# Kernel optimization log

Hardware: AMD Instinct MI355X
Metric: run time of the kernel (lower is better)

Reference implementation:

```python
import jax, jax.numpy as jnp
import numpy as np

D_EMBEDDING = 512
DIMENSION = 64
B, N = 8, 2048


def setup_inputs() -> dict:
    key = jax.random.key(0)
    k1, k2, k3, k4, k5, k6 = jax.random.split(key, 6)
    bound = 1.0 / np.sqrt(D_EMBEDDING)  # nn.Linear default init
    return {
        "key_input": jax.random.normal(k1, (B, N, D_EMBEDDING), jnp.float32),
        "query_input": jax.random.normal(k2, (B, N, D_EMBEDDING), jnp.float32),
        "value_input": jax.random.normal(k3, (B, N, D_EMBEDDING), jnp.float32),
        "padding_mask": jnp.zeros((B, 1, N), dtype=bool),
        "masked_attention": 1,
        "W_key": jax.random.uniform(k4, (D_EMBEDDING, DIMENSION), jnp.float32, -bound, bound),
        "W_query": jax.random.uniform(k5, (D_EMBEDDING, DIMENSION), jnp.float32, -bound, bound),
        "W_value": jax.random.uniform(k6, (D_EMBEDDING, DIMENSION), jnp.float32, -bound, bound),
    }


def reference(key_input, query_input, value_input, padding_mask, masked_attention,
              W_key, W_query, W_value):
    # NOTE: faithful to the original torch code, which uses self.key for
    # Q, K AND V (W_query / W_value are unused by forward) and scales by
    # sqrt(D_i) where D_i is the INPUT embedding dim (512), not the head dim.
    B_, N_, D_i = value_input.shape
    K = key_input @ W_key      # [B, N, d]
    Q = query_input @ W_key    # [B, N, d]
    V = value_input @ W_key    # [B, N, d]

    scores = jnp.einsum("bqd,bkd->bqk", Q, K) / jnp.sqrt(jnp.float32(D_i))
    neg_inf = jnp.float32(-jnp.inf)
    scores = jnp.where(padding_mask, neg_inf, scores)
    if masked_attention:
        causal = jnp.tril(jnp.ones((N_, N_), dtype=bool))  # [N, N]
        scores = jnp.where(causal, scores, neg_inf)
    probs = jax.nn.softmax(scores, axis=-1)
    return jnp.einsum("bqk,bkd->bqd", probs, V)
```

## Files before the change

### kernel.cpp

```cpp
#include <hip/hip_runtime.h>
#include <hip/hip_bf16.h>
#include <math.h>

#define D_EMB 512
#define HD 64
#define BB 8
#define NN 2048
#define MROWS (BB*NN)

typedef short short8  __attribute__((ext_vector_type(8)));
typedef short short4v __attribute__((ext_vector_type(4)));
typedef float f32x4   __attribute__((ext_vector_type(4)));

#define QSCALE 0.063758708f

__device__ __forceinline__ short f2bf(float x){
    unsigned u = __float_as_uint(x);
    unsigned r = (u + 0x7fffu + ((u >> 16) & 1u)) >> 16;
    return (short)r;
}
__device__ __forceinline__ float bf2f(short b){
    return __uint_as_float(((unsigned)(unsigned short)b) << 16);
}
__device__ __forceinline__ unsigned pkbf(float a, float b){
    __hip_bfloat162 h = __float22bfloat162_rn(make_float2(a, b));
    unsigned u; __builtin_memcpy(&u, &h, 4); return u;
}
__device__ __forceinline__ void gl16(const short* g, short* l){
    __builtin_amdgcn_global_load_lds(
        (const __attribute__((address_space(1))) unsigned*)g,
        (__attribute__((address_space(3))) unsigned*)l, 16, 0, 0);
}

__global__ __launch_bounds__(256)
void wt_kernel(const float* __restrict__ W, short* __restrict__ Wtf){
    for (int idx = blockIdx.x * 256 + threadIdx.x; idx < D_EMB*HD; idx += 8*256){
        int k = idx >> 6, n = idx & 63;
        int off = (((k >> 5)*4 + (n >> 4))*64 + ((k >> 3) & 3)*16 + (n & 15))*8 + (k & 7);
        Wtf[off] = f2bf(W[idx]);
    }
}

__global__ __launch_bounds__(256, 4)
void proj_kernel(const float* __restrict__ Xq, const float* __restrict__ Xk,
                 const float* __restrict__ Xv, const short* __restrict__ Wtf,
                 short* __restrict__ Qb, short* __restrict__ Kb,
                 short* __restrict__ Vt)
{
    const int tid = threadIdx.x;
    const int lane = tid & 63;
    const int lc = lane & 15, quad = lane >> 4;
    const int wid = blockIdx.x * 4 + (tid >> 6);
    const int m0 = wid * 16;
    const int tensor = m0 >> 14;
    const int rloc = m0 & (MROWS - 1);
    const float* X = (tensor == 0) ? Xq : (tensor == 1 ? Xk : Xv);
    const float* xbase = X + (size_t)(rloc + lc)*D_EMB + quad*8;

    f32x4 acc[4];
#pragma unroll
    for (int t = 0; t < 4; ++t)
#pragma unroll
        for (int r = 0; r < 4; ++r) acc[t][r] = 0.f;

    float4 xa[4][2];
#pragma unroll
    for (int p = 0; p < 4; ++p){
        xa[p][0] = *(const float4*)(xbase + p*32);
        xa[p][1] = *(const float4*)(xbase + p*32 + 4);
    }
#pragma unroll
    for (int c16 = 0; c16 < 16; ++c16){
        float4 f0 = xa[c16 & 3][0], f1 = xa[c16 & 3][1];
        if (c16 < 12){
            xa[c16 & 3][0] = *(const float4*)(xbase + (c16+4)*32);
            xa[c16 & 3][1] = *(const float4*)(xbase + (c16+4)*32 + 4);
        }
        union { short8 s8; unsigned u[4]; } a;
        a.u[0] = pkbf(f0.x, f0.y); a.u[1] = pkbf(f0.z, f0.w);
        a.u[2] = pkbf(f1.x, f1.y); a.u[3] = pkbf(f1.z, f1.w);
#pragma unroll
        for (int t = 0; t < 4; ++t){
            short8 bf = *(const short8*)(Wtf + (size_t)(((c16*4 + t)*64 + lane)*8));
            acc[t] = __builtin_amdgcn_mfma_f32_16x16x32_bf16(a.s8, bf, acc[t], 0,0,0);
        }
    }

    if (tensor == 0){
#pragma unroll
        for (int t = 0; t < 4; ++t)
#pragma unroll
            for (int r = 0; r < 4; ++r)
                Qb[(size_t)(rloc + quad*4 + r)*HD + t*16 + lc] = f2bf(acc[t][r] * QSCALE);
    } else if (tensor == 1){
#pragma unroll
        for (int t = 0; t < 4; ++t)
#pragma unroll
            for (int r = 0; r < 4; ++r){
                const int R = rloc + quad*4 + r;
                const int nin = R & 63;
                const int off = ((R >> 6) << 12) + nin*64
                              + ((((t << 1) | (lc >> 3)) ^ (nin & 7)) << 3) + (lc & 7);
                Kb[off] = f2bf(acc[t][r]);
            }
    } else {
#pragma unroll
        for (int t = 0; t < 4; ++t)
#pragma unroll
            for (int r = 0; r < 4; ++r){
                const int R = rloc + quad*4 + r;
                const int nin = R & 63;
                const int d = t*16 + lc;
                const int off = ((R >> 6) << 12) + d*64
                              + (((nin >> 3) ^ (lc & 7)) << 3) + (nin & 7);
                Vt[off] = f2bf(acc[t][r]);
            }
    }
}

template<int SH>
__global__ __launch_bounds__(256)
void attn_part(const short* __restrict__ Qb, const short* __restrict__ Kb,
               const short* __restrict__ Vt, const unsigned char* __restrict__ pad,
               const int* __restrict__ mflag, float* __restrict__ out,
               float* __restrict__ Lp, short* __restrict__ Op)
{
    constexpr int M   = 1 << SH;
    constexpr int NG  = 32 / M;
    constexpr int UPB = M * NG * (NG + 1) / 2;
    constexpr int PPB = UPB - M;

    __shared__ short sK[2][4096];
    __shared__ short sV[2][4096];
    __shared__ short sP[4][16][80];

    const int tid = threadIdx.x, lane = tid & 63, lc = lane & 15, quad = lane >> 4, w = tid >> 6;
    const int unit = blockIdx.x;
    const int b = unit / UPB;
    const int rem = unit - b * UPB;
    int a = 0;
    while (rem >= (M * (a + 1) * (a + 2)) / 2) ++a;
    const int u = rem - M * a * (a + 1) / 2;
    const int C = a + 1;
    const int r = u / C, c = u - r * C;
    const int j = a * M + r;
    const int q0 = j * 64;

    const bool causal = (mflag[0] != 0);
    const int T = causal ? (j + 1) : 32;
    const int qq = (T + C - 1) / C;
    const int t0 = c * qq;
    const int t1 = min(t0 + qq, T);
    const int tb = b * 32;
    const unsigned char* padb = pad + (size_t)b * NN;

    const short* qrow = Qb + ((size_t)b * NN + q0 + w*16 + lc) * HD;
    const short8 qf0 = *(const short8*)(qrow + quad * 8);
    const short8 qf1 = *(const short8*)(qrow + 32 + quad * 8);

    f32x4 o[4];
#pragma unroll
    for (int t = 0; t < 4; ++t)
#pragma unroll
        for (int rr = 0; rr < 4; ++rr) o[t][rr] = 0.f;
    float lacc = 0.f;

    {
        const short* gk = Kb + ((size_t)(tb + t0) << 12) + w*1024 + lane*8;
        const short* gv = Vt + ((size_t)(tb + t0) << 12) + w*1024 + lane*8;
        short* lk = &sK[0][w*1024 + lane*8];
        short* lv = &sV[0][w*1024 + lane*8];
        gl16(gk, lk); gl16(gk + 512, lk + 512);
        gl16(gv, lv); gl16(gv + 512, lv + 512);
    }

    int buf = 0;
    const int sw = lc & 7;
    for (int kt = t0; kt < t1; ++kt, buf ^= 1){
        __syncthreads();
        if (kt + 1 < t1){
            const short* gk = Kb + ((size_t)(tb + kt + 1) << 12) + w*1024 + lane*8;
            const short* gv = Vt + ((size_t)(tb + kt + 1) << 12) + w*1024 + lane*8;
            short* lk = &sK[buf ^ 1][w*1024 + lane*8];
            short* lv = &sV[buf ^ 1][w*1024 + lane*8];
            gl16(gk, lk); gl16(gk + 512, lk + 512);
            gl16(gv, lv); gl16(gv + 512, lv + 512);
        }
        const int k0 = kt * 64;
        short8 kf0[4], kf1[4], vf0[4], vf1[4];
#pragma unroll
        for (int t = 0; t < 4; ++t){
            const int row = (t*16 + lc) * 64;
            kf0[t] = *(const short8*)&sK[buf][row + ((quad ^ sw) << 3)];
            kf1[t] = *(const short8*)&sK[buf][row + (((quad + 4) ^ sw) << 3)];
            vf0[t] = *(const short8*)&sV[buf][row + ((quad ^ sw) << 3)];
            vf1[t] = *(const short8*)&sV[buf][row + (((quad + 4) ^ sw) << 3)];
        }
        f32x4 st[4];
#pragma unroll
        for (int t = 0; t < 4; ++t){
#pragma unroll
            for (int rr = 0; rr < 4; ++rr) st[t][rr] = 0.f;
            st[t] = __builtin_amdgcn_mfma_f32_16x16x32_bf16(kf0[t], qf0, st[t], 0,0,0);
            st[t] = __builtin_amdgcn_mfma_f32_16x16x32_bf16(kf1[t], qf1, st[t], 0,0,0);
        }
        const bool dg = causal && (kt == j);
        const int thr = q0 + w*16 + lc - k0;
#pragma unroll
        for (int t = 0; t < 4; ++t){
            uchar4 pb = *(const uchar4*)(padb + k0 + t*16 + quad*4);
            float e[4];
#pragma unroll
            for (int rr = 0; rr < 4; ++rr){
                float v = st[t][rr];
                const unsigned char pr = (rr==0)?pb.x:(rr==1)?pb.y:(rr==2)?pb.z:pb.w;
                const int nloc = t*16 + quad*4 + rr;
                if (pr || (dg && nloc > thr)) v = -INFINITY;
                e[rr] = exp2f(v);
                lacc += e[rr];
            }
            union { short4v s4; unsigned uu[2]; } pk;
            pk.uu[0] = pkbf(e[0], e[1]);
            pk.uu[1] = pkbf(e[2], e[3]);
            *(short4v*)&sP[w][lc][t*16 + quad*4] = pk.s4;
        }
        const short8 pf0 = *(const short8*)&sP[w][lc][quad*8];
        const short8 pf1 = *(const short8*)&sP[w][lc][32 + quad*8];
#pragma unroll
        for (int t = 0; t < 4; ++t){
            o[t] = __builtin_amdgcn_mfma_f32_16x16x32_bf16(pf0, vf0[t], o[t], 0,0,0);
            o[t] = __builtin_amdgcn_mfma_f32_16x16x32_bf16(pf1, vf1[t], o[t], 0,0,0);
        }
    }

    lacc += __shfl_xor(lacc, 16);
    lacc += __shfl_xor(lacc, 32);

    if (C == 1){
        float linv[4];
#pragma unroll
        for (int rr = 0; rr < 4; ++rr) linv[rr] = 1.f / __shfl(lacc, quad*4 + rr);
#pragma unroll
        for (int rr = 0; rr < 4; ++rr){
            float* orow = out + ((size_t)b*NN + q0 + w*16 + quad*4 + rr)*HD;
#pragma unroll
            for (int t = 0; t < 4; ++t) orow[t*16 + lc] = o[t][rr] * linv[rr];
        }
    } else {
        const int pu = b*PPB + (M*a*(a+1)/2 - M) + r*C + c;
        short* op = Op + (size_t)pu * 4096;
#pragma unroll
        for (int t = 0; t < 4; ++t)
#pragma unroll
            for (int rr = 0; rr < 4; ++rr)
                op[(w*16 + quad*4 + rr)*64 + t*16 + lc] = f2bf(o[t][rr]);
        if (lane < 16) Lp[pu*64 + w*16 + lane] = lacc;
    }
}

template<int SH>
__global__ __launch_bounds__(256)
void attn_combine(const float* __restrict__ Lp, const short* __restrict__ Op,
                  float* __restrict__ out)
{
    constexpr int M    = 1 << SH;
    constexpr int UPB  = M * (32/M) * (32/M + 1) / 2;
    constexpr int PPB  = UPB - M;
    constexpr int NSTR = 32 - M;
    const int tid = threadIdx.x, lane = tid & 63;
    const int unit = blockIdx.x;
    const int per_b = NSTR * 16;
    const int b = unit / per_b;
    const int rem = unit - b * per_b;
    const int j = M + (rem >> 4);
    const int row = (rem & 15) * 4 + (tid >> 6);
    const int a = j >> SH;
    const int C = a + 1;
    const int r = j - a * M;
    const int pu0 = b*PPB + (M*a*(a+1)/2 - M) + r*C;

    float l = 0.f, acc = 0.f;
    for (int cc = 0; cc < C; ++cc){
        l   += Lp[(pu0 + cc)*64 + row];
        acc += bf2f(Op[(size_t)(pu0 + cc)*4096 + row*64 + lane]);
    }
    out[((size_t)b*NN + j*64 + row)*HD + lane] = acc / l;
}

extern "C" void kernel_launch(void* const* d_in, const int* in_sizes, int n_in,
                              void* d_out, int out_size, void* d_ws, size_t ws_size,
                              hipStream_t stream) {
    const float* key_in   = (const float*)d_in[0];
    const float* query_in = (const float*)d_in[1];
    const float* value_in = (const float*)d_in[2];
    const unsigned char* pad = (const unsigned char*)d_in[3];
    const int* mflag      = (const int*)d_in[4];
    const float* Wk       = (const float*)d_in[5];

    short* Qb = (short*)d_ws;
    short* Kb = Qb + (size_t)MROWS*HD;
    short* Vt = Kb + (size_t)MROWS*HD;
    short* Wtf = Vt + (size_t)MROWS*HD;
    float* Lp = (float*)(Wtf + D_EMB*HD);

    wt_kernel<<<8, 256, 0, stream>>>(Wk, Wtf);
    proj_kernel<<<768, 256, 0, stream>>>(query_in, key_in, value_in, Wtf, Qb, Kb, Vt);

    if (ws_size >= (size_t)15818752){
        short* Op = (short*)(Lp + 1120*64);
        attn_part<2><<<1152, 256, 0, stream>>>(Qb, Kb, Vt, pad, mflag, (float*)d_out, Lp, Op);
        attn_combine<2><<<BB*28*16, 256, 0, stream>>>(Lp, Op, (float*)d_out);
    } else {
        short* Op = (short*)(Lp + 576*64);
        attn_part<3><<<640, 256, 0, stream>>>(Qb, Kb, Vt, pad, mflag, (float*)d_out, Lp, Op);
        attn_combine<3><<<BB*24*16, 256, 0, stream>>>(Lp, Op, (float*)d_out);
    }
}
```

Baseline: 165.4 us.

## Split projection K-dimension across wave pairs with LDS reduction

The projection kernel now assigns each 16-row tile to a pair of waves, each covering half of the 512-wide input dimension, and reduces their partial accumulators through shared memory. It also issues all eight input loads up front and doubles the grid to 1536 blocks. Separately, the weight transpose kernel is launched with 64 blocks instead of 8. The aim is more memory parallelism in the bandwidth-bound projection, paid for with a __syncthreads, an LDS round-trip, and more registers.

```diff
diff --git a/kernel.cpp b/kernel.cpp
--- a/kernel.cpp
+++ b/kernel.cpp
@@ -34,7 +34,7 @@
 
 __global__ __launch_bounds__(256)
 void wt_kernel(const float* __restrict__ W, short* __restrict__ Wtf){
-    for (int idx = blockIdx.x * 256 + threadIdx.x; idx < D_EMB*HD; idx += 8*256){
+    for (int idx = blockIdx.x * 256 + threadIdx.x; idx < D_EMB*HD; idx += 64*256){
         int k = idx >> 6, n = idx & 63;
         int off = (((k >> 5)*4 + (n >> 4))*64 + ((k >> 3) & 3)*16 + (n & 15))*8 + (k & 7);
         Wtf[off] = f2bf(W[idx]);
@@ -47,43 +47,59 @@
                  short* __restrict__ Qb, short* __restrict__ Kb,
                  short* __restrict__ Vt)
 {
+    __shared__ float sRed[2][64][16];
     const int tid = threadIdx.x;
     const int lane = tid & 63;
     const int lc = lane & 15, quad = lane >> 4;
-    const int wid = blockIdx.x * 4 + (tid >> 6);
-    const int m0 = wid * 16;
+    const int w = tid >> 6;
+    const int pair = w >> 1;
+    const int kh = w & 1;
+    const int grp = blockIdx.x * 2 + pair;
+    const int m0 = grp * 16;
     const int tensor = m0 >> 14;
     const int rloc = m0 & (MROWS - 1);
     const float* X = (tensor == 0) ? Xq : (tensor == 1 ? Xk : Xv);
-    const float* xbase = X + (size_t)(rloc + lc)*D_EMB + quad*8;
-
-    f32x4 acc[4];
-#pragma unroll
-    for (int t = 0; t < 4; ++t)
-#pragma unroll
-        for (int r = 0; r < 4; ++r) acc[t][r] = 0.f;
-
-    float4 xa[4][2];
-#pragma unroll
-    for (int p = 0; p < 4; ++p){
+    const float* xbase = X + (size_t)(rloc + lc)*D_EMB + kh*256 + quad*8;
+
+    float4 xa[8][2];
+#pragma unroll
+    for (int p = 0; p < 8; ++p){
         xa[p][0] = *(const float4*)(xbase + p*32);
         xa[p][1] = *(const float4*)(xbase + p*32 + 4);
     }
-#pragma unroll
-    for (int c16 = 0; c16 < 16; ++c16){
-        float4 f0 = xa[c16 & 3][0], f1 = xa[c16 & 3][1];
-        if (c16 < 12){
-            xa[c16 & 3][0] = *(const float4*)(xbase + (c16+4)*32);
-            xa[c16 & 3][1] = *(const float4*)(xbase + (c16+4)*32 + 4);
-        }
+
+    f32x4 acc[4];
+#pragma unroll
+    for (int t = 0; t < 4; ++t)
+#pragma unroll
+        for (int r = 0; r < 4; ++r) acc[t][r] = 0.f;
+
+#pragma unroll
+    for (int c = 0; c < 8; ++c){
+        const int c16 = kh*8 + c;
         union { short8 s8; unsigned u[4]; } a;
-        a.u[0] = pkbf(f0.x, f0.y); a.u[1] = pkbf(f0.z, f0.w);
-        a.u[2] = pkbf(f1.x, f1.y); a.u[3] = pkbf(f1.z, f1.w);
+        a.u[0] = pkbf(xa[c][0].x, xa[c][0].y); a.u[1] = pkbf(xa[c][0].z, xa[c][0].w);
+        a.u[2] = pkbf(xa[c][1].x, xa[c][1].y); a.u[3] = pkbf(xa[c][1].z, xa[c][1].w);
 #pragma unroll
         for (int t = 0; t < 4; ++t){
             short8 bf = *(const short8*)(Wtf + (size_t)(((c16*4 + t)*64 + lane)*8));
             acc[t] = __builtin_amdgcn_mfma_f32_16x16x32_bf16(a.s8, bf, acc[t], 0,0,0);
         }
+    }
+
+    if (kh == 1){
+#pragma unroll
+        for (int t = 0; t < 4; ++t)
+            *(f32x4*)&sRed[pair][lane][(t ^ (lane & 3))*4] = acc[t];
+    }
+    __syncthreads();
+    if (kh != 0) return;
+
+#pragma unroll
+    for (int t = 0; t < 4; ++t){
+        f32x4 p = *(const f32x4*)&sRed[pair][lane][(t ^ (lane & 3))*4];
+#pragma unroll
+        for (int r = 0; r < 4; ++r) acc[t][r] += p[r];
     }
 
     if (tensor == 0){
@@ -303,8 +319,8 @@
     short* Wtf = Vt + (size_t)MROWS*HD;
     float* Lp = (float*)(Wtf + D_EMB*HD);
 
-    wt_kernel<<<8, 256, 0, stream>>>(Wk, Wtf);
-    proj_kernel<<<768, 256, 0, stream>>>(query_in, key_in, value_in, Wtf, Qb, Kb, Vt);
+    wt_kernel<<<64, 256, 0, stream>>>(Wk, Wtf);
+    proj_kernel<<<1536, 256, 0, stream>>>(query_in, key_in, value_in, Wtf, Qb, Kb, Vt);
 
     if (ws_size >= (size_t)15818752){
         short* Op = (short*)(Lp + 1120*64);
```

Result: no change. 168.0 us (+1.6%).
